# Kernel optimization log

Hardware: AMD Instinct MI355X
Metric: run time of the kernel (lower is better)

Reference implementation:

```python
import jax, jax.numpy as jnp
import numpy as np

N, D, H, C = 100000, 128, 8, 16  # nodes, units=H*C, heads, per-head channels
E = 400000                        # edges per edge set (2 edge sets)
LN_EPS = 1e-3                     # keras LayerNormalization default epsilon


def setup_inputs() -> dict:
    key = jax.random.key(0)
    ks = jax.random.split(key, 16)
    def dense(k, i, o):
        return jax.random.normal(k, (i, o), jnp.float32) / np.float32(np.sqrt(i))
    return dict(
        x=jax.random.normal(ks[0], (N, D), jnp.float32),
        src0=jax.random.randint(ks[1], (E,), 0, N),
        dst0=jax.random.randint(ks[2], (E,), 0, N),
        src1=jax.random.randint(ks[3], (E,), 0, N),
        dst1=jax.random.randint(ks[4], (E,), 0, N),
        Wk=dense(ks[5], D, D), bk=jnp.zeros((D,), jnp.float32),
        Wm=dense(ks[6], D, D), bm=jnp.zeros((D,), jnp.float32),
        Wq=dense(ks[7], D, D), bq=jnp.zeros((D,), jnp.float32),
        Wa=dense(ks[8], D, D), ba=jnp.zeros((D,), jnp.float32),
        Watt0=jax.random.normal(ks[9], (H, C, C), jnp.float32) / np.float32(np.sqrt(C)),
        Wmsg0=jax.random.normal(ks[10], (H, C, C), jnp.float32) / np.float32(np.sqrt(C)),
        Watt1=jax.random.normal(ks[11], (H, C, C), jnp.float32) / np.float32(np.sqrt(C)),
        Wmsg1=jax.random.normal(ks[12], (H, C, C), jnp.float32) / np.float32(np.sqrt(C)),
        prior0=jnp.ones((H,), jnp.float32),
        prior1=jnp.ones((H,), jnp.float32),
        skip=jnp.ones((), jnp.float32),
        gamma=jnp.ones((D,), jnp.float32),
        beta=jnp.zeros((D,), jnp.float32),
    )


def reference(x, src0, dst0, src1, dst1, Wk, bk, Wm, bm, Wq, bq, Wa, ba,
              Watt0, Wmsg0, Watt1, Wmsg1, prior0, prior1, skip, gamma, beta):
    # Node-level projections, split per head: [N, H, C]
    k = (x @ Wk + bk).reshape(N, H, C)
    m = (x @ Wm + bm).reshape(N, H, C)
    q = (x @ Wq + bq).reshape(N, H, C)
    scale = 1.0 / jnp.sqrt(jnp.float32(C))

    def edge_terms(src, dst, Watt, Wmsg, prior):
        # per-edge-type relation projections of gathered sender keys/messages
        ke = jnp.einsum('ehk,hkl->ehl', k[src], Watt)          # [E, H, C]
        score = jnp.einsum('ehl,ehl->eh', ke, q[dst]) * prior * scale  # [E, H]
        msg = jnp.einsum('ehk,hkl->ehl', m[src], Wmsg)          # [E, H, C]
        return score, msg

    s0, m0 = edge_terms(src0, dst0, Watt0, Wmsg0, prior0)
    s1, m1 = edge_terms(src1, dst1, Watt1, Wmsg1, prior1)

    # Joint segment softmax over all incoming edges (both edge sets) per receiver
    scores = jnp.concatenate([s0, s1], axis=0)   # [2E, H]
    msgs = jnp.concatenate([m0, m1], axis=0)     # [2E, H, C]
    recv = jnp.concatenate([dst0, dst1], axis=0)

    smax = jax.ops.segment_max(scores, recv, num_segments=N)   # [N, H]
    ex = jnp.exp(scores - smax[recv])
    denom = jax.ops.segment_sum(ex, recv, num_segments=N)      # [N, H]
    d_e = denom[recv]
    attn = ex / jnp.where(d_e > 0, d_e, 1.0)                   # [2E, H]

    pooled = jax.ops.segment_sum(attn[:, :, None] * msgs, recv,
                                 num_segments=N).reshape(N, D)  # [N, D]

    # aggr(gelu(pooled)); weighted skip; layer norm
    h = jax.nn.gelu(pooled, approximate=False) @ Wa + ba
    alpha = jax.nn.sigmoid(skip)
    out = alpha * h + (1.0 - alpha) * x
    mu = jnp.mean(out, axis=-1, keepdims=True)
    var = jnp.var(out, axis=-1, keepdims=True)
    out = (out - mu) * jax.lax.rsqrt(var + LN_EPS) * gamma + beta
    return out
```

## Files before the change

kernel.cpp:

```cpp
#include <hip/hip_runtime.h>
#include <hip/hip_bf16.h>
#include <math.h>

#define N_NODES 100000
#define DIM 128
#define NH 8
#define NC 16
#define E_EDGES 400000
#define LN_EPS 1e-3f
#define SCAN_B 1024
#define PROJ_GRID 512

typedef __attribute__((ext_vector_type(8))) short short8v;
typedef __attribute__((ext_vector_type(4))) short short4v;
typedef __attribute__((ext_vector_type(4))) float float4v;

__device__ __forceinline__ short bf16bits(float v) {
    __hip_bfloat16 b = __float2bfloat16(v);
    return *(short*)&b;
}

__device__ __forceinline__ void bf2x2(unsigned v, float& a, float& b) {
    a = __uint_as_float(v << 16);
    b = __uint_as_float(v & 0xffff0000u);
}

__global__ __launch_bounds__(128) void fuse_weights(
    const float* __restrict__ Wk, const float* __restrict__ bk,
    const float* __restrict__ Wm, const float* __restrict__ bm,
    const float* __restrict__ Wq, const float* __restrict__ bq,
    const float* __restrict__ Wa, const float* __restrict__ ba,
    const float* __restrict__ Watt0, const float* __restrict__ Wmsg0,
    const float* __restrict__ Watt1, const float* __restrict__ Wmsg1,
    const float* __restrict__ prior0, const float* __restrict__ prior1,
    __hip_bfloat16* __restrict__ Wt, float* __restrict__ bias)
{
    const int c = blockIdx.x;
    const int d = threadIdx.x;
    const int sec = c >> 7, j = c & 127, h = j >> 4, l = j & 15;
    float v, b;
    if (sec == 4)      { v = Wq[d * DIM + j]; b = bq[j]; }
    else if (sec == 5) { v = Wa[d * DIM + j]; b = ba[j]; }
    else {
        const float* W1 = (sec < 2) ? Wk : Wm;
        const float* bs = (sec < 2) ? bk : bm;
        const float* W2 = (sec == 0) ? Watt0 : (sec == 1) ? Watt1
                          : (sec == 2) ? Wmsg0 : Wmsg1;
        float scale = (sec == 0) ? prior0[h] * 0.25f
                    : (sec == 1) ? prior1[h] * 0.25f : 1.f;
        float s = 0.f, sb = 0.f;
        #pragma unroll
        for (int kk = 0; kk < NC; ++kk) {
            float w2 = W2[h * 256 + kk * 16 + l];
            s  = fmaf(W1[d * DIM + h * 16 + kk], w2, s);
            sb = fmaf(bs[h * 16 + kk], w2, sb);
        }
        v = s * scale; b = sb * scale;
    }
    Wt[(size_t)c * DIM + d] = __float2bfloat16(v);
    if (d == 0) bias[c] = b;
}

__global__ __launch_bounds__(512) void proj_mfma(
    const float* __restrict__ x,
    const __hip_bfloat16* __restrict__ Wt,
    const float* __restrict__ bias,
    __hip_bfloat16* __restrict__ km,
    __hip_bfloat16* __restrict__ qb)
{
    __shared__ __align__(16) short xs[2][32 * DIM];
    const int tid = threadIdx.x;
    const int wave = tid >> 6, lane = tid & 63;
    const int quad = lane >> 4, mcol = lane & 15;
    const int nt = N_NODES / 32;

    short8v wf[5][4];
    float4v bv[5];
    #pragma unroll
    for (int s = 0; s < 5; ++s) {
        const int c0 = s * 128 + wave * 16;
        const short* wp = (const short*)Wt + (size_t)(c0 + mcol) * DIM + quad * 8;
        #pragma unroll
        for (int kb = 0; kb < 4; ++kb)
            wf[s][kb] = *(const short8v*)(wp + kb * 32);
        bv[s] = *(const float4v*)(bias + c0 + quad * 4);
    }

    const int srow = tid >> 4, sc8 = tid & 15;
    const int swz = ((sc8 ^ (srow & 7)) * 8);

    int t = blockIdx.x;
    if (t >= nt) return;

    float4v f0 = *(const float4v*)(x + (size_t)(t * 32 + srow) * DIM + sc8 * 8);
    float4v f1 = *(const float4v*)(x + (size_t)(t * 32 + srow) * DIM + sc8 * 8 + 4);
    {
        short8v sv;
        #pragma unroll
        for (int j = 0; j < 4; ++j) { sv[j] = bf16bits(f0[j]); sv[j + 4] = bf16bits(f1[j]); }
        *(short8v*)(xs[0] + srow * DIM + swz) = sv;
    }
    {
        int nn = t + PROJ_GRID;
        if (nn < nt) {
            f0 = *(const float4v*)(x + (size_t)(nn * 32 + srow) * DIM + sc8 * 8);
            f1 = *(const float4v*)(x + (size_t)(nn * 32 + srow) * DIM + sc8 * 8 + 4);
        }
    }

    int cur = 0;
    for (; t < nt; t += PROJ_GRID) {
        asm volatile("s_waitcnt lgkmcnt(0)" ::: "memory");
        __builtin_amdgcn_s_barrier();

        short8v b0[4], b1[4];
        #pragma unroll
        for (int kb = 0; kb < 4; ++kb) {
            const int ch = ((quad + kb * 4) ^ (mcol & 7)) * 8;
            b0[kb] = *(const short8v*)(xs[cur] + mcol * DIM + ch);
            b1[kb] = *(const short8v*)(xs[cur] + (mcol + 16) * DIM + ch);
        }

        const int r0 = t * 32;

        #pragma unroll
        for (int e = 0; e < 2; ++e) {
            float4v aK0 = {0.f,0.f,0.f,0.f}, aK1 = {0.f,0.f,0.f,0.f};
            float4v aM0 = {0.f,0.f,0.f,0.f}, aM1 = {0.f,0.f,0.f,0.f};
            #pragma unroll
            for (int kb = 0; kb < 4; ++kb) {
                aK0 = __builtin_amdgcn_mfma_f32_16x16x32_bf16(wf[e][kb],     b0[kb], aK0, 0, 0, 0);
                aK1 = __builtin_amdgcn_mfma_f32_16x16x32_bf16(wf[e][kb],     b1[kb], aK1, 0, 0, 0);
                aM0 = __builtin_amdgcn_mfma_f32_16x16x32_bf16(wf[2 + e][kb], b0[kb], aM0, 0, 0, 0);
                aM1 = __builtin_amdgcn_mfma_f32_16x16x32_bf16(wf[2 + e][kb], b1[kb], aM1, 0, 0, 0);
            }
            short8v o0, o1;
            #pragma unroll
            for (int g = 0; g < 4; ++g) {
                o0[g]     = bf16bits(aK0[g] + bv[e][g]);
                o0[g + 4] = bf16bits(aM0[g] + bv[2 + e][g]);
                o1[g]     = bf16bits(aK1[g] + bv[e][g]);
                o1[g + 4] = bf16bits(aM1[g] + bv[2 + e][g]);
            }
            short* dp = (short*)km
                      + ((size_t)(r0 + mcol) + (size_t)e * N_NODES) * 256
                      + (wave * 4 + quad) * 8;
            *(short8v*)dp              = o0;
            *(short8v*)(dp + 16 * 256) = o1;
        }

        {
            float4v a0v = {0.f,0.f,0.f,0.f}, a1v = {0.f,0.f,0.f,0.f};
            #pragma unroll
            for (int kb = 0; kb < 4; ++kb) {
                a0v = __builtin_amdgcn_mfma_f32_16x16x32_bf16(wf[4][kb], b0[kb], a0v, 0, 0, 0);
                a1v = __builtin_amdgcn_mfma_f32_16x16x32_bf16(wf[4][kb], b1[kb], a1v, 0, 0, 0);
            }
            short4v o0, o1;
            #pragma unroll
            for (int g = 0; g < 4; ++g) {
                o0[g] = bf16bits(a0v[g] + bv[4][g]);
                o1[g] = bf16bits(a1v[g] + bv[4][g]);
            }
            short* dp = (short*)qb + (size_t)(r0 + mcol) * DIM + wave * 16 + quad * 4;
            *(short4v*)dp              = o0;
            *(short4v*)(dp + 16 * DIM) = o1;
        }

        int nn = t + PROJ_GRID;
        if (nn < nt) {
            short8v sv;
            #pragma unroll
            for (int j = 0; j < 4; ++j) { sv[j] = bf16bits(f0[j]); sv[j + 4] = bf16bits(f1[j]); }
            *(short8v*)(xs[cur ^ 1] + srow * DIM + swz) = sv;
            int n2 = nn + PROJ_GRID;
            if (n2 < nt) {
                f0 = *(const float4v*)(x + (size_t)(n2 * 32 + srow) * DIM + sc8 * 8);
                f1 = *(const float4v*)(x + (size_t)(n2 * 32 + srow) * DIM + sc8 * 8 + 4);
            }
        }
        cur ^= 1;
    }
}

__global__ __launch_bounds__(256) void hist_kernel(
    const int* __restrict__ dst0, const int* __restrict__ dst1,
    int* __restrict__ counts)
{
    int e = blockIdx.x * 256 + threadIdx.x;
    if (e < E_EDGES) atomicAdd(&counts[dst0[e]], 1);
    int e1 = e - E_EDGES;
    if (e1 >= 0 && e1 < E_EDGES) atomicAdd(&counts[dst1[e1]], 1);
}

__global__ __launch_bounds__(SCAN_B) void scanA_kernel(
    const int* __restrict__ counts, int* __restrict__ row_ptr,
    int* __restrict__ bsum)
{
    __shared__ int buf[2][SCAN_B];
    int i = blockIdx.x * SCAN_B + threadIdx.x;
    int v = (i < N_NODES) ? counts[i] : 0;
    int cur = 0;
    buf[0][threadIdx.x] = v;
    __syncthreads();
    #pragma unroll
    for (int off = 1; off < SCAN_B; off <<= 1) {
        int t = buf[cur][threadIdx.x];
        int add = (threadIdx.x >= off) ? buf[cur][threadIdx.x - off] : 0;
        buf[cur ^ 1][threadIdx.x] = t + add;
        cur ^= 1;
        __syncthreads();
    }
    int inc = buf[cur][threadIdx.x];
    if (i < N_NODES) row_ptr[i] = inc - v;
    if (threadIdx.x == SCAN_B - 1) bsum[blockIdx.x] = inc;
}

__global__ __launch_bounds__(128) void scanB_kernel(int* __restrict__ bsum, int nblocks)
{
    __shared__ int buf[2][128];
    int t = threadIdx.x;
    int v = (t < nblocks) ? bsum[t] : 0;
    buf[0][t] = v;
    __syncthreads();
    int cur = 0;
    #pragma unroll
    for (int off = 1; off < 128; off <<= 1) {
        int a = buf[cur][t];
        if (t >= off) a += buf[cur][t - off];
        buf[cur ^ 1][t] = a;
        cur ^= 1;
        __syncthreads();
    }
    if (t < nblocks) bsum[t] = buf[cur][t] - v;
}

__global__ __launch_bounds__(SCAN_B) void scanC_kernel(
    int* __restrict__ row_ptr, int* __restrict__ cursor,
    const int* __restrict__ bsum)
{
    int i = blockIdx.x * SCAN_B + threadIdx.x;
    if (i < N_NODES) {
        int r = row_ptr[i] + bsum[blockIdx.x];
        row_ptr[i] = r;
        cursor[i] = r;
    }
}

__global__ __launch_bounds__(256) void scatter_kernel(
    const int* __restrict__ src0, const int* __restrict__ dst0,
    const int* __restrict__ src1, const int* __restrict__ dst1,
    int* __restrict__ cursor, unsigned int* __restrict__ eidx)
{
    int e = blockIdx.x * 256 + threadIdx.x;
    if (e < E_EDGES) {
        int d = dst0[e];
        int pos = atomicAdd(&cursor[d], 1);
        eidx[pos] = (unsigned int)src0[e];
    }
    int e1 = e - E_EDGES;
    if (e1 >= 0 && e1 < E_EDGES) {
        int d = dst1[e1];
        int pos = atomicAdd(&cursor[d], 1);
        eidx[pos] = (unsigned int)(src1[e1] + N_NODES);
    }
}

__global__ __launch_bounds__(256) void agg_kernel(
    const char* __restrict__ km,
    const uint2* __restrict__ qv,
    const int* __restrict__ row_ptr, const int* __restrict__ counts,
    const unsigned int* __restrict__ eidx,
    uint2* __restrict__ pooled)
{
    const int wave = threadIdx.x >> 6, lane = threadIdx.x & 63;
    const int n = blockIdx.x * 4 + wave;
    if (n >= N_NODES) return;
    const int start = row_ptr[n], cnt = counts[n];
    const int hi = lane >> 5;
    const int glane = lane & 31;
    const unsigned g16 = (unsigned)glane << 4;

    uint2 qu = qv[(size_t)n * 32 + glane];
    float q0, q1, q2, q3;
    bf2x2(qu.x, q0, q1); bf2x2(qu.y, q2, q3);

    float a0 = 0.f, a1 = 0.f, a2 = 0.f, a3 = 0.f, den = 0.f;

#define PAIR_ACC(u)                                                          \
    {                                                                        \
        float k0, k1, k2, k3, m0, m1, m2, m3;                                \
        bf2x2((u).x, k0, k1); bf2x2((u).y, k2, k3);                          \
        bf2x2((u).z, m0, m1); bf2x2((u).w, m2, m3);                          \
        float p = fmaf(k3, q3, fmaf(k2, q2, fmaf(k1, q1, k0 * q0)));         \
        p += __shfl_xor(p, 1, 64);                                           \
        p += __shfl_xor(p, 2, 64);                                           \
        float e = __expf(p);                                                 \
        den += e;                                                            \
        a0 = fmaf(e, m0, a0); a1 = fmaf(e, m1, a1);                          \
        a2 = fmaf(e, m2, a2); a3 = fmaf(e, m3, a3);                          \
    }

    int i = 0;
    for (; i + 8 <= cnt; i += 8) {
        unsigned ra = eidx[start + i + hi];
        unsigned rb = eidx[start + i + 2 + hi];
        unsigned rc = eidx[start + i + 4 + hi];
        unsigned rd = eidx[start + i + 6 + hi];
        uint4 ua = *(const uint4*)(km + (((size_t)ra << 9) | g16));
        uint4 ub = *(const uint4*)(km + (((size_t)rb << 9) | g16));
        uint4 uc = *(const uint4*)(km + (((size_t)rc << 9) | g16));
        uint4 ud = *(const uint4*)(km + (((size_t)rd << 9) | g16));
        PAIR_ACC(ua); PAIR_ACC(ub); PAIR_ACC(uc); PAIR_ACC(ud);
    }
    for (; i + 2 <= cnt; i += 2) {
        unsigned ra = eidx[start + i + hi];
        uint4 ua = *(const uint4*)(km + (((size_t)ra << 9) | g16));
        PAIR_ACC(ua);
    }
    if (i < cnt) {
        unsigned ra = eidx[start + i];
        uint4 ua = *(const uint4*)(km + (((size_t)ra << 9) | g16));
        float k0, k1, k2, k3, m0, m1, m2, m3;
        bf2x2(ua.x, k0, k1); bf2x2(ua.y, k2, k3);
        bf2x2(ua.z, m0, m1); bf2x2(ua.w, m2, m3);
        float p = fmaf(k3, q3, fmaf(k2, q2, fmaf(k1, q1, k0 * q0)));
        p += __shfl_xor(p, 1, 64);
        p += __shfl_xor(p, 2, 64);
        float e = hi ? 0.f : __expf(p);
        den += e;
        a0 = fmaf(e, m0, a0); a1 = fmaf(e, m1, a1);
        a2 = fmaf(e, m2, a2); a3 = fmaf(e, m3, a3);
    }
#undef PAIR_ACC

    den += __shfl_xor(den, 32, 64);
    a0 += __shfl_xor(a0, 32, 64);
    a1 += __shfl_xor(a1, 32, 64);
    a2 += __shfl_xor(a2, 32, 64);
    a3 += __shfl_xor(a3, 32, 64);

    float inv = (den > 0.f) ? (1.f / den) : 0.f;
    float v0 = a0 * inv, v1 = a1 * inv, v2 = a2 * inv, v3 = a3 * inv;

    float s0 = hi ? v2 : v0;
    float s1 = hi ? v3 : v1;
    s0 = 0.5f * s0 * (1.f + erff(s0 * 0.70710678118654752f));
    s1 = 0.5f * s1 * (1.f + erff(s1 * 0.70710678118654752f));
    unsigned pk = ((unsigned)(unsigned short)bf16bits(s0))
                | ((unsigned)(unsigned short)bf16bits(s1) << 16);
    unsigned ph = __shfl_xor(pk, 32, 64);
    if (!hi) {
        uint2 o; o.x = pk; o.y = ph;
        pooled[(size_t)n * 32 + glane] = o;
    }
}

__global__ __launch_bounds__(256) void final_mfma(
    const __hip_bfloat16* __restrict__ pooled,
    const __hip_bfloat16* __restrict__ Wt,
    const float* __restrict__ bias,
    const float* __restrict__ x,
    const float* __restrict__ skip, const float* __restrict__ gamma,
    const float* __restrict__ beta, float* __restrict__ out)
{
    __shared__ float hs[32][DIM];
    const int wave = threadIdx.x >> 6, lane = threadIdx.x & 63;
    const int quad = lane >> 4, mcol = lane & 15;
    const int r0 = blockIdx.x * 32;

    short8v a0[4], a1[4];
    const short* pp0 = (const short*)pooled + (size_t)(r0 + mcol) * DIM + quad * 8;
    const short* pp1 = pp0 + 16 * DIM;
    #pragma unroll
    for (int kb = 0; kb < 4; ++kb) {
        a0[kb] = *(const short8v*)(pp0 + kb * 32);
        a1[kb] = *(const short8v*)(pp1 + kb * 32);
    }
    const float alpha = 1.f / (1.f + expf(-skip[0]));

    #pragma unroll
    for (int t = 0; t < 2; ++t) {
        const int c0 = wave * 32 + t * 16;
        const short* wp = (const short*)Wt + (size_t)(640 + c0 + mcol) * DIM + quad * 8;
        float4v acc0 = {0.f, 0.f, 0.f, 0.f};
        float4v acc1 = {0.f, 0.f, 0.f, 0.f};
        #pragma unroll
        for (int kb = 0; kb < 4; ++kb) {
            short8v bfr = *(const short8v*)(wp + kb * 32);
            acc0 = __builtin_amdgcn_mfma_f32_16x16x32_bf16(a0[kb], bfr, acc0, 0, 0, 0);
            acc1 = __builtin_amdgcn_mfma_f32_16x16x32_bf16(a1[kb], bfr, acc1, 0, 0, 0);
        }
        const float bcol = bias[640 + c0 + mcol];
        const int cc = c0 + mcol;
        const int rq = quad * 4;
        #pragma unroll
        for (int g = 0; g < 4; ++g) {
            int rA = rq + g, rB = rq + 16 + g;
            hs[rA][cc] = alpha * (acc0[g] + bcol)
                       + (1.f - alpha) * x[(size_t)(r0 + rA) * DIM + cc];
            hs[rB][cc] = alpha * (acc1[g] + bcol)
                       + (1.f - alpha) * x[(size_t)(r0 + rB) * DIM + cc];
        }
    }
    __syncthreads();

    float gam0 = gamma[lane], gam1 = gamma[lane + 64];
    float bet0 = beta[lane],  bet1 = beta[lane + 64];
    for (int r = wave; r < 32; r += 4) {
        int row = r0 + r;
        float v0 = hs[r][lane], v1 = hs[r][lane + 64];
        float s = v0 + v1, s2 = v0 * v0 + v1 * v1;
        #pragma unroll
        for (int off = 1; off < 64; off <<= 1) {
            s  += __shfl_xor(s,  off, 64);
            s2 += __shfl_xor(s2, off, 64);
        }
        float mu = s * (1.f / 128.f);
        float var = s2 * (1.f / 128.f) - mu * mu;
        float rstd = rsqrtf(var + LN_EPS);
        out[(size_t)row * DIM + lane]      = (v0 - mu) * rstd * gam0 + bet0;
        out[(size_t)row * DIM + lane + 64] = (v1 - mu) * rstd * gam1 + bet1;
    }
}

extern "C" void kernel_launch(void* const* d_in, const int* in_sizes, int n_in,
                              void* d_out, int out_size, void* d_ws, size_t ws_size,
                              hipStream_t stream) {
    const float* x     = (const float*)d_in[0];
    const int*   src0  = (const int*)d_in[1];
    const int*   dst0  = (const int*)d_in[2];
    const int*   src1  = (const int*)d_in[3];
    const int*   dst1  = (const int*)d_in[4];
    const float* Wk    = (const float*)d_in[5];
    const float* bk    = (const float*)d_in[6];
    const float* Wm    = (const float*)d_in[7];
    const float* bm    = (const float*)d_in[8];
    const float* Wq    = (const float*)d_in[9];
    const float* bq    = (const float*)d_in[10];
    const float* Wa    = (const float*)d_in[11];
    const float* ba    = (const float*)d_in[12];
    const float* Watt0 = (const float*)d_in[13];
    const float* Wmsg0 = (const float*)d_in[14];
    const float* Watt1 = (const float*)d_in[15];
    const float* Wmsg1 = (const float*)d_in[16];
    const float* prior0= (const float*)d_in[17];
    const float* prior1= (const float*)d_in[18];
    const float* skip  = (const float*)d_in[19];
    const float* gamma = (const float*)d_in[20];
    const float* beta  = (const float*)d_in[21];
    float* out = (float*)d_out;

    const size_t nd = (size_t)N_NODES * DIM;
    char* wsb = (char*)d_ws;
    __hip_bfloat16* Wt    = (__hip_bfloat16*)wsb;  wsb += (size_t)768 * DIM * 2;
    float* bias           = (float*)wsb;           wsb += 768 * 4;
    __hip_bfloat16* km    = (__hip_bfloat16*)wsb;  wsb += (size_t)2 * N_NODES * 256 * 2;
    __hip_bfloat16* qb    = (__hip_bfloat16*)wsb;  wsb += nd * 2;
    __hip_bfloat16* pooled= (__hip_bfloat16*)wsb;  wsb += nd * 2;
    int* counts  = (int*)wsb;                      wsb += (size_t)N_NODES * 4;
    int* row_ptr = (int*)wsb;                      wsb += (size_t)N_NODES * 4;
    int* cursor  = (int*)wsb;                      wsb += (size_t)N_NODES * 4;
    int* bsum    = (int*)wsb;                      wsb += 128 * 4;
    unsigned int* eidx = (unsigned int*)wsb;

    hipMemsetAsync(counts, 0, (size_t)N_NODES * 4, stream);

    const int scan_blocks = (N_NODES + SCAN_B - 1) / SCAN_B;
    const int edge_blocks = (2 * E_EDGES + 255) / 256;

    hist_kernel<<<dim3(edge_blocks), dim3(256), 0, stream>>>(dst0, dst1, counts);
    scanA_kernel<<<dim3(scan_blocks), dim3(SCAN_B), 0, stream>>>(counts, row_ptr, bsum);
    scanB_kernel<<<dim3(1), dim3(128), 0, stream>>>(bsum, scan_blocks);
    scanC_kernel<<<dim3(scan_blocks), dim3(SCAN_B), 0, stream>>>(row_ptr, cursor, bsum);
    scatter_kernel<<<dim3(edge_blocks), dim3(256), 0, stream>>>(
        src0, dst0, src1, dst1, cursor, eidx);

    fuse_weights<<<dim3(768), dim3(128), 0, stream>>>(
        Wk, bk, Wm, bm, Wq, bq, Wa, ba,
        Watt0, Wmsg0, Watt1, Wmsg1, prior0, prior1, Wt, bias);
    proj_mfma<<<dim3(PROJ_GRID), dim3(512), 0, stream>>>(
        x, Wt, bias, km, qb);

    agg_kernel<<<dim3((N_NODES + 3) / 4), dim3(256), 0, stream>>>(
        (const char*)km, (const uint2*)qb, row_ptr, counts, eidx,
        (uint2*)pooled);

    final_mfma<<<dim3(N_NODES / 32), dim3(256), 0, stream>>>(
        pooled, Wt, bias, x, skip, gamma, beta, out);
}
```

Baseline: 354.6 us.

## Move relation weights to query side and apply Wmsg after aggregation

The per-edge-type relation matrices are folded into the query projection: Watt is applied to q (two q variants per node), and Wmsg is applied after pooling through a block-diagonal matrix in the final kernel. Edges now gather one shared raw k/m row per source instead of one of two type-specific rows, which halves the gathered table and improves cache reuse in aggregation. Edge type is stored in the top bit of the edge index. In exchange, the aggregation keeps two per-type accumulators and writes a 256-wide pooled buffer, and the final kernel runs an extra 256x128 MFMA stage with GELU and an LDS round trip.

```diff
diff --git a/kernel.cpp b/kernel.cpp
--- a/kernel.cpp
+++ b/kernel.cpp
@@ -38,24 +38,25 @@
     const int c = blockIdx.x;
     const int d = threadIdx.x;
     const int sec = c >> 7, j = c & 127, h = j >> 4, l = j & 15;
-    float v, b;
-    if (sec == 4)      { v = Wq[d * DIM + j]; b = bq[j]; }
-    else if (sec == 5) { v = Wa[d * DIM + j]; b = ba[j]; }
-    else {
-        const float* W1 = (sec < 2) ? Wk : Wm;
-        const float* bs = (sec < 2) ? bk : bm;
-        const float* W2 = (sec == 0) ? Watt0 : (sec == 1) ? Watt1
-                          : (sec == 2) ? Wmsg0 : Wmsg1;
-        float scale = (sec == 0) ? prior0[h] * 0.25f
-                    : (sec == 1) ? prior1[h] * 0.25f : 1.f;
+    float v = 0.f, b = 0.f;
+    if (sec == 0)      { v = Wk[d * DIM + j]; b = bk[j]; }
+    else if (sec == 1) { v = Wm[d * DIM + j]; b = bm[j]; }
+    else if (sec == 4) { v = Wa[d * DIM + j]; b = ba[j]; }
+    else if (sec == 2 || sec == 3) {
+        const float* W2 = (sec == 2) ? Watt0 : Watt1;
+        float scale = ((sec == 2) ? prior0[h] : prior1[h]) * 0.25f;
         float s = 0.f, sb = 0.f;
         #pragma unroll
-        for (int kk = 0; kk < NC; ++kk) {
-            float w2 = W2[h * 256 + kk * 16 + l];
-            s  = fmaf(W1[d * DIM + h * 16 + kk], w2, s);
-            sb = fmaf(bs[h * 16 + kk], w2, sb);
+        for (int ll = 0; ll < NC; ++ll) {
+            float w2 = W2[h * 256 + l * 16 + ll];
+            s  = fmaf(Wq[d * DIM + h * 16 + ll], w2, s);
+            sb = fmaf(bq[h * 16 + ll], w2, sb);
         }
         v = s * scale; b = sb * scale;
+    } else {
+        const float* W2 = (sec == 5) ? Wmsg0 : Wmsg1;
+        v = ((d >> 4) == h) ? W2[h * 256 + (d & 15) * 16 + l] : 0.f;
+        b = 0.f;
     }
     Wt[(size_t)c * DIM + d] = __float2bfloat16(v);
     if (d == 0) bias[c] = b;
@@ -65,8 +66,8 @@
     const float* __restrict__ x,
     const __hip_bfloat16* __restrict__ Wt,
     const float* __restrict__ bias,
-    __hip_bfloat16* __restrict__ km,
-    __hip_bfloat16* __restrict__ qb)
+    __hip_bfloat16* __restrict__ kmr,
+    __hip_bfloat16* __restrict__ qe)
 {
     __shared__ __align__(16) short xs[2][32 * DIM];
     const int tid = threadIdx.x;
@@ -74,10 +75,10 @@
     const int quad = lane >> 4, mcol = lane & 15;
     const int nt = N_NODES / 32;
 
-    short8v wf[5][4];
-    float4v bv[5];
-    #pragma unroll
-    for (int s = 0; s < 5; ++s) {
+    short8v wf[4][4];
+    float4v bv[4];
+    #pragma unroll
+    for (int s = 0; s < 4; ++s) {
         const int c0 = s * 128 + wave * 16;
         const short* wp = (const short*)Wt + (size_t)(c0 + mcol) * DIM + quad * 8;
         #pragma unroll
@@ -123,46 +124,46 @@
 
         const int r0 = t * 32;
 
-        #pragma unroll
-        for (int e = 0; e < 2; ++e) {
+        {
             float4v aK0 = {0.f,0.f,0.f,0.f}, aK1 = {0.f,0.f,0.f,0.f};
             float4v aM0 = {0.f,0.f,0.f,0.f}, aM1 = {0.f,0.f,0.f,0.f};
             #pragma unroll
             for (int kb = 0; kb < 4; ++kb) {
-                aK0 = __builtin_amdgcn_mfma_f32_16x16x32_bf16(wf[e][kb],     b0[kb], aK0, 0, 0, 0);
-                aK1 = __builtin_amdgcn_mfma_f32_16x16x32_bf16(wf[e][kb],     b1[kb], aK1, 0, 0, 0);
-                aM0 = __builtin_amdgcn_mfma_f32_16x16x32_bf16(wf[2 + e][kb], b0[kb], aM0, 0, 0, 0);
-                aM1 = __builtin_amdgcn_mfma_f32_16x16x32_bf16(wf[2 + e][kb], b1[kb], aM1, 0, 0, 0);
+                aK0 = __builtin_amdgcn_mfma_f32_16x16x32_bf16(wf[0][kb], b0[kb], aK0, 0, 0, 0);
+                aK1 = __builtin_amdgcn_mfma_f32_16x16x32_bf16(wf[0][kb], b1[kb], aK1, 0, 0, 0);
+                aM0 = __builtin_amdgcn_mfma_f32_16x16x32_bf16(wf[1][kb], b0[kb], aM0, 0, 0, 0);
+                aM1 = __builtin_amdgcn_mfma_f32_16x16x32_bf16(wf[1][kb], b1[kb], aM1, 0, 0, 0);
             }
             short8v o0, o1;
             #pragma unroll
             for (int g = 0; g < 4; ++g) {
-                o0[g]     = bf16bits(aK0[g] + bv[e][g]);
-                o0[g + 4] = bf16bits(aM0[g] + bv[2 + e][g]);
-                o1[g]     = bf16bits(aK1[g] + bv[e][g]);
-                o1[g + 4] = bf16bits(aM1[g] + bv[2 + e][g]);
+                o0[g]     = bf16bits(aK0[g] + bv[0][g]);
+                o0[g + 4] = bf16bits(aM0[g] + bv[1][g]);
+                o1[g]     = bf16bits(aK1[g] + bv[0][g]);
+                o1[g + 4] = bf16bits(aM1[g] + bv[1][g]);
             }
-            short* dp = (short*)km
-                      + ((size_t)(r0 + mcol) + (size_t)e * N_NODES) * 256
+            short* dp = (short*)kmr + (size_t)(r0 + mcol) * 256
                       + (wave * 4 + quad) * 8;
             *(short8v*)dp              = o0;
             *(short8v*)(dp + 16 * 256) = o1;
         }
 
-        {
+        #pragma unroll
+        for (int e = 0; e < 2; ++e) {
             float4v a0v = {0.f,0.f,0.f,0.f}, a1v = {0.f,0.f,0.f,0.f};
             #pragma unroll
             for (int kb = 0; kb < 4; ++kb) {
-                a0v = __builtin_amdgcn_mfma_f32_16x16x32_bf16(wf[4][kb], b0[kb], a0v, 0, 0, 0);
-                a1v = __builtin_amdgcn_mfma_f32_16x16x32_bf16(wf[4][kb], b1[kb], a1v, 0, 0, 0);
+                a0v = __builtin_amdgcn_mfma_f32_16x16x32_bf16(wf[2 + e][kb], b0[kb], a0v, 0, 0, 0);
+                a1v = __builtin_amdgcn_mfma_f32_16x16x32_bf16(wf[2 + e][kb], b1[kb], a1v, 0, 0, 0);
             }
             short4v o0, o1;
             #pragma unroll
             for (int g = 0; g < 4; ++g) {
-                o0[g] = bf16bits(a0v[g] + bv[4][g]);
-                o1[g] = bf16bits(a1v[g] + bv[4][g]);
+                o0[g] = bf16bits(a0v[g] + bv[2 + e][g]);
+                o1[g] = bf16bits(a1v[g] + bv[2 + e][g]);
             }
-            short* dp = (short*)qb + (size_t)(r0 + mcol) * DIM + wave * 16 + quad * 4;
+            short* dp = (short*)qe + ((size_t)e * N_NODES + r0 + mcol) * DIM
+                      + wave * 16 + quad * 4;
             *(short4v*)dp              = o0;
             *(short4v*)(dp + 16 * DIM) = o1;
         }
@@ -262,16 +263,16 @@
     if (e1 >= 0 && e1 < E_EDGES) {
         int d = dst1[e1];
         int pos = atomicAdd(&cursor[d], 1);
-        eidx[pos] = (unsigned int)(src1[e1] + N_NODES);
+        eidx[pos] = (unsigned int)src1[e1] | 0x80000000u;
     }
 }
 
 __global__ __launch_bounds__(256) void agg_kernel(
-    const char* __restrict__ km,
-    const uint2* __restrict__ qv,
+    const char* __restrict__ kmr,
+    const uint2* __restrict__ qe,
     const int* __restrict__ row_ptr, const int* __restrict__ counts,
     const unsigned int* __restrict__ eidx,
-    uint2* __restrict__ pooled)
+    __hip_bfloat16* __restrict__ acc)
 {
     const int wave = threadIdx.x >> 6, lane = threadIdx.x & 63;
     const int n = blockIdx.x * 4 + wave;
@@ -281,24 +282,33 @@
     const int glane = lane & 31;
     const unsigned g16 = (unsigned)glane << 4;
 
-    uint2 qu = qv[(size_t)n * 32 + glane];
-    float q0, q1, q2, q3;
-    bf2x2(qu.x, q0, q1); bf2x2(qu.y, q2, q3);
-
-    float a0 = 0.f, a1 = 0.f, a2 = 0.f, a3 = 0.f, den = 0.f;
-
-#define PAIR_ACC(u)                                                          \
+    uint2 qu0 = qe[(size_t)n * 32 + glane];
+    uint2 qu1 = qe[((size_t)N_NODES + n) * 32 + glane];
+    float q00, q01, q02, q03, q10, q11, q12, q13;
+    bf2x2(qu0.x, q00, q01); bf2x2(qu0.y, q02, q03);
+    bf2x2(qu1.x, q10, q11); bf2x2(qu1.y, q12, q13);
+
+    float b0 = 0.f, b1 = 0.f, b2 = 0.f, b3 = 0.f;
+    float c0 = 0.f, c1 = 0.f, c2 = 0.f, c3 = 0.f;
+    float den = 0.f;
+
+#define PAIR_ACC(u, s1)                                                      \
     {                                                                        \
         float k0, k1, k2, k3, m0, m1, m2, m3;                                \
         bf2x2((u).x, k0, k1); bf2x2((u).y, k2, k3);                          \
         bf2x2((u).z, m0, m1); bf2x2((u).w, m2, m3);                          \
-        float p = fmaf(k3, q3, fmaf(k2, q2, fmaf(k1, q1, k0 * q0)));         \
+        float qa = (s1) ? q10 : q00, qb = (s1) ? q11 : q01;                  \
+        float qc = (s1) ? q12 : q02, qd = (s1) ? q13 : q03;                  \
+        float p = fmaf(k3, qd, fmaf(k2, qc, fmaf(k1, qb, k0 * qa)));         \
         p += __shfl_xor(p, 1, 64);                                           \
         p += __shfl_xor(p, 2, 64);                                           \
         float e = __expf(p);                                                 \
         den += e;                                                            \
-        a0 = fmaf(e, m0, a0); a1 = fmaf(e, m1, a1);                          \
-        a2 = fmaf(e, m2, a2); a3 = fmaf(e, m3, a3);                          \
+        float e0 = (s1) ? 0.f : e, e1s = (s1) ? e : 0.f;                     \
+        b0 = fmaf(e0, m0, b0); b1 = fmaf(e0, m1, b1);                        \
+        b2 = fmaf(e0, m2, b2); b3 = fmaf(e0, m3, b3);                        \
+        c0 = fmaf(e1s, m0, c0); c1 = fmaf(e1s, m1, c1);                      \
+        c2 = fmaf(e1s, m2, c2); c3 = fmaf(e1s, m3, c3);                      \
     }
 
     int i = 0;
@@ -307,73 +317,80 @@
         unsigned rb = eidx[start + i + 2 + hi];
         unsigned rc = eidx[start + i + 4 + hi];
         unsigned rd = eidx[start + i + 6 + hi];
-        uint4 ua = *(const uint4*)(km + (((size_t)ra << 9) | g16));
-        uint4 ub = *(const uint4*)(km + (((size_t)rb << 9) | g16));
-        uint4 uc = *(const uint4*)(km + (((size_t)rc << 9) | g16));
-        uint4 ud = *(const uint4*)(km + (((size_t)rd << 9) | g16));
-        PAIR_ACC(ua); PAIR_ACC(ub); PAIR_ACC(uc); PAIR_ACC(ud);
+        uint4 ua = *(const uint4*)(kmr + ((size_t)(ra & 0x7fffffffu) << 9 | g16));
+        uint4 ub = *(const uint4*)(kmr + ((size_t)(rb & 0x7fffffffu) << 9 | g16));
+        uint4 uc = *(const uint4*)(kmr + ((size_t)(rc & 0x7fffffffu) << 9 | g16));
+        uint4 ud = *(const uint4*)(kmr + ((size_t)(rd & 0x7fffffffu) << 9 | g16));
+        PAIR_ACC(ua, (ra >> 31));
+        PAIR_ACC(ub, (rb >> 31));
+        PAIR_ACC(uc, (rc >> 31));
+        PAIR_ACC(ud, (rd >> 31));
     }
     for (; i + 2 <= cnt; i += 2) {
         unsigned ra = eidx[start + i + hi];
-        uint4 ua = *(const uint4*)(km + (((size_t)ra << 9) | g16));
-        PAIR_ACC(ua);
+        uint4 ua = *(const uint4*)(kmr + ((size_t)(ra & 0x7fffffffu) << 9 | g16));
+        PAIR_ACC(ua, (ra >> 31));
     }
     if (i < cnt) {
         unsigned ra = eidx[start + i];
-        uint4 ua = *(const uint4*)(km + (((size_t)ra << 9) | g16));
+        uint4 ua = *(const uint4*)(kmr + ((size_t)(ra & 0x7fffffffu) << 9 | g16));
+        unsigned s1 = ra >> 31;
         float k0, k1, k2, k3, m0, m1, m2, m3;
         bf2x2(ua.x, k0, k1); bf2x2(ua.y, k2, k3);
         bf2x2(ua.z, m0, m1); bf2x2(ua.w, m2, m3);
-        float p = fmaf(k3, q3, fmaf(k2, q2, fmaf(k1, q1, k0 * q0)));
+        float qa = s1 ? q10 : q00, qb = s1 ? q11 : q01;
+        float qc = s1 ? q12 : q02, qd = s1 ? q13 : q03;
+        float p = fmaf(k3, qd, fmaf(k2, qc, fmaf(k1, qb, k0 * qa)));
         p += __shfl_xor(p, 1, 64);
         p += __shfl_xor(p, 2, 64);
         float e = hi ? 0.f : __expf(p);
         den += e;
-        a0 = fmaf(e, m0, a0); a1 = fmaf(e, m1, a1);
-        a2 = fmaf(e, m2, a2); a3 = fmaf(e, m3, a3);
+        float e0 = s1 ? 0.f : e, e1s = s1 ? e : 0.f;
+        b0 = fmaf(e0, m0, b0); b1 = fmaf(e0, m1, b1);
+        b2 = fmaf(e0, m2, b2); b3 = fmaf(e0, m3, b3);
+        c0 = fmaf(e1s, m0, c0); c1 = fmaf(e1s, m1, c1);
+        c2 = fmaf(e1s, m2, c2); c3 = fmaf(e1s, m3, c3);
     }
 #undef PAIR_ACC
 
     den += __shfl_xor(den, 32, 64);
-    a0 += __shfl_xor(a0, 32, 64);
-    a1 += __shfl_xor(a1, 32, 64);
-    a2 += __shfl_xor(a2, 32, 64);
-    a3 += __shfl_xor(a3, 32, 64);
+    b0 += __shfl_xor(b0, 32, 64); b1 += __shfl_xor(b1, 32, 64);
+    b2 += __shfl_xor(b2, 32, 64); b3 += __shfl_xor(b3, 32, 64);
+    c0 += __shfl_xor(c0, 32, 64); c1 += __shfl_xor(c1, 32, 64);
+    c2 += __shfl_xor(c2, 32, 64); c3 += __shfl_xor(c3, 32, 64);
 
     float inv = (den > 0.f) ? (1.f / den) : 0.f;
-    float v0 = a0 * inv, v1 = a1 * inv, v2 = a2 * inv, v3 = a3 * inv;
-
-    float s0 = hi ? v2 : v0;
-    float s1 = hi ? v3 : v1;
-    s0 = 0.5f * s0 * (1.f + erff(s0 * 0.70710678118654752f));
-    s1 = 0.5f * s1 * (1.f + erff(s1 * 0.70710678118654752f));
-    unsigned pk = ((unsigned)(unsigned short)bf16bits(s0))
-                | ((unsigned)(unsigned short)bf16bits(s1) << 16);
-    unsigned ph = __shfl_xor(pk, 32, 64);
+    short4v o;
     if (!hi) {
-        uint2 o; o.x = pk; o.y = ph;
-        pooled[(size_t)n * 32 + glane] = o;
+        o[0] = bf16bits(b0 * inv); o[1] = bf16bits(b1 * inv);
+        o[2] = bf16bits(b2 * inv); o[3] = bf16bits(b3 * inv);
+        *(short4v*)((short*)acc + (size_t)n * 256 + glane * 4) = o;
+    } else {
+        o[0] = bf16bits(c0 * inv); o[1] = bf16bits(c1 * inv);
+        o[2] = bf16bits(c2 * inv); o[3] = bf16bits(c3 * inv);
+        *(short4v*)((short*)acc + (size_t)n * 256 + 128 + glane * 4) = o;
     }
 }
 
 __global__ __launch_bounds__(256) void final_mfma(
-    const __hip_bfloat16* __restrict__ pooled,
+    const __hip_bfloat16* __restrict__ acc,
     const __hip_bfloat16* __restrict__ Wt,
     const float* __restrict__ bias,
     const float* __restrict__ x,
     const float* __restrict__ skip, const float* __restrict__ gamma,
     const float* __restrict__ beta, float* __restrict__ out)
 {
+    __shared__ __align__(16) short Pl[32 * DIM];
     __shared__ float hs[32][DIM];
     const int wave = threadIdx.x >> 6, lane = threadIdx.x & 63;
     const int quad = lane >> 4, mcol = lane & 15;
     const int r0 = blockIdx.x * 32;
 
-    short8v a0[4], a1[4];
-    const short* pp0 = (const short*)pooled + (size_t)(r0 + mcol) * DIM + quad * 8;
-    const short* pp1 = pp0 + 16 * DIM;
-    #pragma unroll
-    for (int kb = 0; kb < 4; ++kb) {
+    short8v a0[8], a1[8];
+    const short* pp0 = (const short*)acc + (size_t)(r0 + mcol) * 256 + quad * 8;
+    const short* pp1 = pp0 + 16 * 256;
+    #pragma unroll
+    for (int kb = 0; kb < 8; ++kb) {
         a0[kb] = *(const short8v*)(pp0 + kb * 32);
         a1[kb] = *(const short8v*)(pp1 + kb * 32);
     }
@@ -382,16 +399,56 @@
     #pragma unroll
     for (int t = 0; t < 2; ++t) {
         const int c0 = wave * 32 + t * 16;
-        const short* wp = (const short*)Wt + (size_t)(640 + c0 + mcol) * DIM + quad * 8;
+        const short* wp5 = (const short*)Wt + (size_t)(5 * 128 + c0 + mcol) * DIM + quad * 8;
+        const short* wp6 = (const short*)Wt + (size_t)(6 * 128 + c0 + mcol) * DIM + quad * 8;
+        float4v p0 = {0.f, 0.f, 0.f, 0.f};
+        float4v p1 = {0.f, 0.f, 0.f, 0.f};
+        #pragma unroll
+        for (int kb = 0; kb < 4; ++kb) {
+            short8v bfr = *(const short8v*)(wp5 + kb * 32);
+            p0 = __builtin_amdgcn_mfma_f32_16x16x32_bf16(a0[kb], bfr, p0, 0, 0, 0);
+            p1 = __builtin_amdgcn_mfma_f32_16x16x32_bf16(a1[kb], bfr, p1, 0, 0, 0);
+        }
+        #pragma unroll
+        for (int kb = 0; kb < 4; ++kb) {
+            short8v bfr = *(const short8v*)(wp6 + kb * 32);
+            p0 = __builtin_amdgcn_mfma_f32_16x16x32_bf16(a0[kb + 4], bfr, p0, 0, 0, 0);
+            p1 = __builtin_amdgcn_mfma_f32_16x16x32_bf16(a1[kb + 4], bfr, p1, 0, 0, 0);
+        }
+        const int cc = c0 + mcol;
+        #pragma unroll
+        for (int g = 0; g < 4; ++g) {
+            int rA = quad * 4 + g, rB = rA + 16;
+            float vA = p0[g], vB = p1[g];
+            vA = 0.5f * vA * (1.f + erff(vA * 0.70710678118654752f));
+            vB = 0.5f * vB * (1.f + erff(vB * 0.70710678118654752f));
+            Pl[rA * DIM + (((cc >> 3) ^ (rA & 7)) << 3) + (cc & 7)] = bf16bits(vA);
+            Pl[rB * DIM + (((cc >> 3) ^ (rB & 7)) << 3) + (cc & 7)] = bf16bits(vB);
+        }
+    }
+    __syncthreads();
+
+    short8v g0[4], g1[4];
+    #pragma unroll
+    for (int kb = 0; kb < 4; ++kb) {
+        const int ch = quad + kb * 4;
+        g0[kb] = *(const short8v*)(Pl + mcol * DIM + ((ch ^ (mcol & 7)) << 3));
+        g1[kb] = *(const short8v*)(Pl + (mcol + 16) * DIM + ((ch ^ (mcol & 7)) << 3));
+    }
+
+    #pragma unroll
+    for (int t = 0; t < 2; ++t) {
+        const int c0 = wave * 32 + t * 16;
+        const short* wp = (const short*)Wt + (size_t)(4 * 128 + c0 + mcol) * DIM + quad * 8;
         float4v acc0 = {0.f, 0.f, 0.f, 0.f};
         float4v acc1 = {0.f, 0.f, 0.f, 0.f};
         #pragma unroll
         for (int kb = 0; kb < 4; ++kb) {
             short8v bfr = *(const short8v*)(wp + kb * 32);
-            acc0 = __builtin_amdgcn_mfma_f32_16x16x32_bf16(a0[kb], bfr, acc0, 0, 0, 0);
-            acc1 = __builtin_amdgcn_mfma_f32_16x16x32_bf16(a1[kb], bfr, acc1, 0, 0, 0);
-        }
-        const float bcol = bias[640 + c0 + mcol];
+            acc0 = __builtin_amdgcn_mfma_f32_16x16x32_bf16(g0[kb], bfr, acc0, 0, 0, 0);
+            acc1 = __builtin_amdgcn_mfma_f32_16x16x32_bf16(g1[kb], bfr, acc1, 0, 0, 0);
+        }
+        const float bcol = bias[512 + c0 + mcol];
         const int cc = c0 + mcol;
         const int rq = quad * 4;
         #pragma unroll
@@ -451,13 +508,12 @@
     const float* beta  = (const float*)d_in[21];
     float* out = (float*)d_out;
 
-    const size_t nd = (size_t)N_NODES * DIM;
     char* wsb = (char*)d_ws;
-    __hip_bfloat16* Wt    = (__hip_bfloat16*)wsb;  wsb += (size_t)768 * DIM * 2;
-    float* bias           = (float*)wsb;           wsb += 768 * 4;
-    __hip_bfloat16* km    = (__hip_bfloat16*)wsb;  wsb += (size_t)2 * N_NODES * 256 * 2;
-    __hip_bfloat16* qb    = (__hip_bfloat16*)wsb;  wsb += nd * 2;
-    __hip_bfloat16* pooled= (__hip_bfloat16*)wsb;  wsb += nd * 2;
+    __hip_bfloat16* Wt    = (__hip_bfloat16*)wsb;  wsb += (size_t)896 * DIM * 2;
+    float* bias           = (float*)wsb;           wsb += 896 * 4;
+    __hip_bfloat16* kmr   = (__hip_bfloat16*)wsb;  wsb += (size_t)N_NODES * 256 * 2;
+    __hip_bfloat16* qe    = (__hip_bfloat16*)wsb;  wsb += (size_t)2 * N_NODES * DIM * 2;
+    __hip_bfloat16* acc   = (__hip_bfloat16*)wsb;  wsb += (size_t)N_NODES * 256 * 2;
     int* counts  = (int*)wsb;                      wsb += (size_t)N_NODES * 4;
     int* row_ptr = (int*)wsb;                      wsb += (size_t)N_NODES * 4;
     int* cursor  = (int*)wsb;                      wsb += (size_t)N_NODES * 4;
@@ -476,16 +532,15 @@
     scatter_kernel<<<dim3(edge_blocks), dim3(256), 0, stream>>>(
         src0, dst0, src1, dst1, cursor, eidx);
 
-    fuse_weights<<<dim3(768), dim3(128), 0, stream>>>(
+    fuse_weights<<<dim3(896), dim3(128), 0, stream>>>(
         Wk, bk, Wm, bm, Wq, bq, Wa, ba,
         Watt0, Wmsg0, Watt1, Wmsg1, prior0, prior1, Wt, bias);
     proj_mfma<<<dim3(PROJ_GRID), dim3(512), 0, stream>>>(
-        x, Wt, bias, km, qb);
+        x, Wt, bias, kmr, qe);
 
     agg_kernel<<<dim3((N_NODES + 3) / 4), dim3(256), 0, stream>>>(
-        (const char*)km, (const uint2*)qb, row_ptr, counts, eidx,
-        (uint2*)pooled);
+        (const char*)kmr, (const uint2*)qe, row_ptr, counts, eidx, acc);
 
     final_mfma<<<dim3(N_NODES / 32), dim3(256), 0, stream>>>(
-        pooled, Wt, bias, x, skip, gamma, beta, out);
-}
+        acc, Wt, bias, x, skip, gamma, beta, out);
+}
```

New measurement: 393.6 us. 1.11x slower.
